# Kernel tuning notes

Measured on AMD Instinct MI355X. Metric: run time of the kernel, lower is better.

The kernel has to match this reference:

```python
import jax, jax.numpy as jnp
import numpy as np

N = 8192
FEAT = 3
TRIG = 2
SA = 2
H = 64
ACT = 3
NEG = -1.0e9
EPS = 1e-5


def setup_inputs() -> dict:
    key = jax.random.key(0)
    ks = jax.random.split(key, 24)
    s = 0.05
    node_features = jax.random.uniform(ks[0], (N, FEAT), dtype=jnp.float32)
    adj = jax.random.randint(ks[1], (N, N), 0, 2).astype(jnp.float32)
    # ensure self-loops so every row has at least one neighbor
    adj_matrix = jnp.maximum(adj, jnp.eye(N, dtype=jnp.float32))
    trigger_context = jax.random.uniform(ks[2], (TRIG,), dtype=jnp.float32)
    sa_priors = jax.random.normal(ks[3], (N, SA), dtype=jnp.float32)
    p = lambda k, sh: jax.random.normal(k, sh, dtype=jnp.float32) * s
    return {
        "node_features": node_features,
        "adj_matrix": adj_matrix,
        "trigger_context": trigger_context,
        "sa_priors": sa_priors,
        # node_encoder: Linear(5,64) -> ReLU -> Linear(64,64)
        "w1": p(ks[4], (FEAT + TRIG, H)), "b1": jnp.zeros((H,), jnp.float32),
        "w2": p(ks[5], (H, H)), "b2": jnp.zeros((H,), jnp.float32),
        "wq": p(ks[6], (H, H)), "bq": jnp.zeros((H,), jnp.float32),
        "wk": p(ks[7], (H, H)), "bk": jnp.zeros((H,), jnp.float32),
        "wg": p(ks[8], (TRIG, H)), "bg": jnp.zeros((H,), jnp.float32),
        "stateful_bias": jnp.zeros((1,), jnp.float32),
        "wm": p(ks[9], (H, H)), "bm": jnp.zeros((H,), jnp.float32),
        "ln_g": jnp.ones((H,), jnp.float32), "ln_b": jnp.zeros((H,), jnp.float32),
        "wa1": p(ks[10], (H + SA, H)), "ba1": jnp.zeros((H,), jnp.float32),
        "wa2": p(ks[11], (H, ACT)), "ba2": jnp.zeros((ACT,), jnp.float32),
    }


def reference(node_features, adj_matrix, trigger_context, sa_priors,
              w1, b1, w2, b2, wq, bq, wk, bk, wg, bg, stateful_bias,
              wm, bm, ln_g, ln_b, wa1, ba1, wa2, ba2):
    n = node_features.shape[0]
    trig = jnp.broadcast_to(trigger_context[None, :], (n, TRIG))
    x = jnp.concatenate([node_features, trig], axis=1)          # [N, 5]
    h = jax.nn.relu(x @ w1 + b1) @ w2 + b2                       # [N, H]
    q = h @ wq + bq
    k = h @ wk + bk
    scores = (q @ k.T) * (1.0 / np.sqrt(H))                      # [N, N]
    gate_factor = jnp.mean(jax.nn.sigmoid(trigger_context @ wg + bg))
    topo = jnp.where(adj_matrix == 0, jnp.float32(NEG), adj_matrix)
    is_stateful = node_features[:, 2]
    is_reactive = 1.0 - trigger_context[0]
    sb = jnp.outer(is_stateful, is_stateful) * (stateful_bias[0] * is_reactive)
    scores = scores * gate_factor + topo + sb
    attn = jax.nn.softmax(scores, axis=1)                        # [N, N]
    messages = h @ wm + bm
    aggregated = attn @ messages                                 # [N, H]
    z = h + aggregated
    mu = jnp.mean(z, axis=-1, keepdims=True)
    var = jnp.mean(jnp.square(z - mu), axis=-1, keepdims=True)
    emb = (z - mu) * jax.lax.rsqrt(var + EPS) * ln_g + ln_b      # LayerNorm
    ai = jnp.concatenate([emb, sa_priors], axis=1)               # [N, H+2]
    q_values = jax.nn.relu(ai @ wa1 + ba1) @ wa2 + ba2           # [N, 3]
    return q_values
```

## Files before the change

kernel.cpp:

```cpp
#include <hip/hip_runtime.h>
#include <hip/hip_bf16.h>
#include <math.h>

#define N 8192
#define NEGV -1000000000.0f
#define EPSV 1e-05f
#define NSPLIT 8
#define CPS (N / NSPLIT)
#define NTILE (CPS / 64)

typedef short bf16x8 __attribute__((ext_vector_type(8)));
typedef float f32x4 __attribute__((ext_vector_type(4)));
typedef unsigned short u16;
typedef unsigned int u32;

#define WS_SCAL 0
#define WS_H    64
#define WS_ST   (WS_H + N * 64)
#define WS_SBI  (WS_ST + N)
#define WS_DEN  (WS_SBI + N)
#define WS_AGG  (WS_DEN + NSPLIT * N)
#define WS_F_END (WS_AGG + NSPLIT * N * 64)
#define WU_BASE (WS_F_END * 2)
#define WU_QB (WU_BASE)
#define WU_KB (WU_BASE + N * 64)
#define WU_MB (WU_BASE + 2 * N * 64)
#define WU_MT (WU_BASE + 3 * N * 64)

static __device__ __forceinline__ u16 f2bf(float f) {
    __hip_bfloat16 h = __float2bfloat16(f);
    return *(u16*)&h;
}
static __device__ __forceinline__ u32 pk2(float a, float b) {
    return (u32)f2bf(a) | ((u32)f2bf(b) << 16);
}

__global__ void prep_k(const float* __restrict__ tc, const float* __restrict__ wg,
                       const float* __restrict__ bg, const float* __restrict__ sbias,
                       float* __restrict__ scal) {
    int j = threadIdx.x;
    float v = tc[0] * wg[j] + tc[1] * wg[64 + j] + bg[j];
    float g = 1.0f / (1.0f + __expf(-v));
    for (int off = 32; off; off >>= 1) g += __shfl_xor(g, off, 64);
    if (j == 0) {
        scal[0] = 0.125f * (g * (1.0f / 64.0f));
        scal[1] = sbias[0] * (1.0f - tc[0]);
    }
}

__global__ __launch_bounds__(256) void embed_k(
    const float* __restrict__ nf, const float* __restrict__ tc,
    const float* __restrict__ w1, const float* __restrict__ b1,
    const float* __restrict__ w2, const float* __restrict__ b2,
    const float* __restrict__ wq, const float* __restrict__ bq,
    const float* __restrict__ wk, const float* __restrict__ bk,
    const float* __restrict__ wm, const float* __restrict__ bm,
    float* __restrict__ ws)
{
    const int w = threadIdx.x >> 6, lane = threadIdx.x & 63;
    const int row = blockIdx.x * 4 + w;
    __shared__ float ts[4][64], hs[4][64];
    const float qscale = ws[WS_SCAL + 0];
    const float coef   = ws[WS_SCAL + 1];
    const float f0 = nf[row * 3], f1 = nf[row * 3 + 1], f2 = nf[row * 3 + 2];
    const float t0 = tc[0], t1 = tc[1];
    float v = b1[lane];
    v = fmaf(f0, w1[lane], v);
    v = fmaf(f1, w1[64 + lane], v);
    v = fmaf(f2, w1[128 + lane], v);
    v = fmaf(t0, w1[192 + lane], v);
    v = fmaf(t1, w1[256 + lane], v);
    ts[w][lane] = fmaxf(v, 0.0f);
    __syncthreads();
    float hv = b2[lane];
    #pragma unroll 8
    for (int j = 0; j < 64; j++) hv = fmaf(ts[w][j], w2[j * 64 + lane], hv);
    hs[w][lane] = hv;
    ws[WS_H + row * 64 + lane] = hv;
    __syncthreads();
    float qv = bq[lane], kv = bk[lane], mv = bm[lane];
    #pragma unroll 4
    for (int j = 0; j < 64; j++) {
        const float hj = hs[w][j];
        qv = fmaf(hj, wq[j * 64 + lane], qv);
        kv = fmaf(hj, wk[j * 64 + lane], kv);
        mv = fmaf(hj, wm[j * 64 + lane], mv);
    }
    u16* wu = (u16*)ws;
    wu[WU_QB + row * 64 + lane] = f2bf(qv * qscale);
    wu[WU_KB + row * 64 + lane] = f2bf(kv);
    wu[WU_MB + row * 64 + lane] = f2bf(mv);
    if (lane == 0) {
        ws[WS_ST + row]  = f2;
        ws[WS_SBI + row] = f2 * coef;
    }
}

__global__ __launch_bounds__(256) void transp_k(float* __restrict__ ws) {
    const u16* mb = (const u16*)ws + WU_MB;
    u16* mt = (u16*)ws + WU_MT;
    __shared__ __align__(16) u16 tile[64][72];
    const int i0 = blockIdx.x * 64;
    const int t = threadIdx.x;
    {
        const int r = t >> 2, cb = (t & 3) * 16;
        *(uint4*)&tile[r][cb]     = *(const uint4*)&mb[(size_t)(i0 + r) * 64 + cb];
        *(uint4*)&tile[r][cb + 8] = *(const uint4*)&mb[(size_t)(i0 + r) * 64 + cb + 8];
    }
    __syncthreads();
    const int c = t >> 2, rb = (t & 3) * 16;
    u16 tmp[16];
    #pragma unroll
    for (int i = 0; i < 16; i++) tmp[i] = tile[rb + i][c];
    *(uint4*)&mt[(size_t)c * N + i0 + rb]     = *(uint4*)&tmp[0];
    *(uint4*)&mt[(size_t)c * N + i0 + rb + 8] = *(uint4*)&tmp[8];
}

__global__ __launch_bounds__(256, 4) void attn_k(const float* __restrict__ adj,
                                                 float* __restrict__ ws)
{
    const int rb = blockIdx.x, sp = blockIdx.y;
    const int i0 = rb * 64, j0 = sp * CPS;
    const int tid = threadIdx.x;
    const int w = tid >> 6, lane = tid & 63;
    const int quad = lane >> 4, n16 = lane & 15;
    const int m0 = w * 16;

    __shared__ __align__(16) u16 ps[4][16][72];

    const u16* qb = (const u16*)ws + WU_QB;
    const u16* kb = (const u16*)ws + WU_KB;
    const u16* mt = (const u16*)ws + WU_MT;

    const u16* qr = qb + (size_t)(i0 + m0 + n16) * 64;
    const bf16x8 aq0 = *(const bf16x8*)&qr[quad * 8];
    const bf16x8 aq1 = *(const bf16x8*)&qr[32 + quad * 8];

    const float sbr = ws[WS_SBI + i0 + m0 + n16];
    const float* adjrow = adj + (size_t)(i0 + m0 + n16) * N;

    f32x4 acc[4];
    #pragma unroll
    for (int i = 0; i < 4; i++) acc[i] = (f32x4){0.f, 0.f, 0.f, 0.f};
    float den = 0.0f;

    f32x4 a4[4];
    #pragma unroll
    for (int ct = 0; ct < 4; ct++)
        a4[ct] = *(const f32x4*)&adjrow[j0 + ct * 16 + quad * 4];

    for (int t = 0; t < NTILE; t++) {
        const int jt = j0 + t * 64;

        f32x4 a4n[4];
        if (t + 1 < NTILE) {
            const int jn = jt + 64;
            #pragma unroll
            for (int ct = 0; ct < 4; ct++)
                a4n[ct] = *(const f32x4*)&adjrow[jn + ct * 16 + quad * 4];
        }

        #pragma unroll
        for (int ct = 0; ct < 4; ct++) {
            const u16* kr = kb + (size_t)(jt + ct * 16 + n16) * 64;
            const bf16x8 k0 = *(const bf16x8*)&kr[quad * 8];
            const bf16x8 k1 = *(const bf16x8*)&kr[32 + quad * 8];
            f32x4 s = {0.f, 0.f, 0.f, 0.f};
            s = __builtin_amdgcn_mfma_f32_16x16x32_bf16(k0, aq0, s, 0, 0, 0);
            s = __builtin_amdgcn_mfma_f32_16x16x32_bf16(k1, aq1, s, 0, 0, 0);
            const f32x4 sv = *(const f32x4*)&ws[WS_ST + jt + ct * 16 + quad * 4];
            const f32x4 av = a4[ct];
            float pv[4];
            #pragma unroll
            for (int r = 0; r < 4; r++) {
                const float e = av[r] * __expf(fmaf(sbr, sv[r], s[r]));
                den += e;
                pv[r] = e;
            }
            *(uint2*)&ps[w][n16][ct * 16 + quad * 4] =
                make_uint2(pk2(pv[0], pv[1]), pk2(pv[2], pv[3]));
        }

        const bf16x8 ap0 = *(const bf16x8*)&ps[w][n16][quad * 8];
        const bf16x8 ap1 = *(const bf16x8*)&ps[w][n16][32 + quad * 8];
        #pragma unroll
        for (int nt = 0; nt < 4; nt++) {
            const u16* mr = mt + (size_t)(nt * 16 + n16) * N + jt;
            const bf16x8 b0 = *(const bf16x8*)&mr[quad * 8];
            const bf16x8 b1 = *(const bf16x8*)&mr[32 + quad * 8];
            acc[nt] = __builtin_amdgcn_mfma_f32_16x16x32_bf16(ap0, b0, acc[nt], 0, 0, 0);
            acc[nt] = __builtin_amdgcn_mfma_f32_16x16x32_bf16(ap1, b1, acc[nt], 0, 0, 0);
        }

        #pragma unroll
        for (int ct = 0; ct < 4; ct++) a4[ct] = a4n[ct];
    }

    float* aggp = ws + WS_AGG + (size_t)sp * N * 64;
    #pragma unroll
    for (int nt = 0; nt < 4; nt++) {
        #pragma unroll
        for (int reg = 0; reg < 4; reg++) {
            aggp[(size_t)(i0 + m0 + quad * 4 + reg) * 64 + nt * 16 + n16] = acc[nt][reg];
        }
    }
    den += __shfl_xor(den, 16, 64);
    den += __shfl_xor(den, 32, 64);
    if (quad == 0) ws[WS_DEN + sp * N + i0 + m0 + n16] = den;
}

__global__ __launch_bounds__(256) void final_k(
    const float* __restrict__ sa, const float* __restrict__ ln_g,
    const float* __restrict__ ln_b,
    const float* __restrict__ wa1, const float* __restrict__ ba1,
    const float* __restrict__ wa2, const float* __restrict__ ba2,
    const float* __restrict__ ws, float* __restrict__ out)
{
    const int w = threadIdx.x >> 6, lane = threadIdx.x & 63;
    const int row = blockIdx.x * 4 + w;
    __shared__ float es[4][64], hs2[4][64];
    float a = 0.0f;
    #pragma unroll
    for (int sp = 0; sp < NSPLIT; sp++)
        a += ws[WS_AGG + (size_t)sp * N * 64 + (size_t)row * 64 + lane];
    float d = 0.0f;
    #pragma unroll
    for (int sp = 0; sp < NSPLIT; sp++) d += ws[WS_DEN + sp * N + row];
    const float z = ws[WS_H + row * 64 + lane] + a / d;
    float mu = z;
    for (int off = 32; off; off >>= 1) mu += __shfl_xor(mu, off, 64);
    mu *= (1.0f / 64.0f);
    const float zc = z - mu;
    float var = zc * zc;
    for (int off = 32; off; off >>= 1) var += __shfl_xor(var, off, 64);
    var *= (1.0f / 64.0f);
    const float emb = zc * rsqrtf(var + EPSV) * ln_g[lane] + ln_b[lane];
    es[w][lane] = emb;
    __syncthreads();
    const float sa0 = sa[row * 2], sa1 = sa[row * 2 + 1];
    float hv = ba1[lane];
    #pragma unroll 8
    for (int c = 0; c < 64; c++) hv = fmaf(es[w][c], wa1[c * 64 + lane], hv);
    hv = fmaf(sa0, wa1[64 * 64 + lane], hv);
    hv = fmaf(sa1, wa1[65 * 64 + lane], hv);
    hs2[w][lane] = fmaxf(hv, 0.0f);
    __syncthreads();
    if (lane < 3) {
        float o = ba2[lane];
        for (int u = 0; u < 64; u++) o = fmaf(hs2[w][u], wa2[u * 3 + lane], o);
        out[row * 3 + lane] = o;
    }
}

extern "C" void kernel_launch(void* const* d_in, const int* in_sizes, int n_in,
                              void* d_out, int out_size, void* d_ws, size_t ws_size,
                              hipStream_t stream)
{
    const float* nf  = (const float*)d_in[0];
    const float* adj = (const float*)d_in[1];
    const float* tc  = (const float*)d_in[2];
    const float* sa  = (const float*)d_in[3];
    const float* w1  = (const float*)d_in[4];
    const float* b1  = (const float*)d_in[5];
    const float* w2  = (const float*)d_in[6];
    const float* b2  = (const float*)d_in[7];
    const float* wq  = (const float*)d_in[8];
    const float* bq  = (const float*)d_in[9];
    const float* wk  = (const float*)d_in[10];
    const float* bk  = (const float*)d_in[11];
    const float* wg  = (const float*)d_in[12];
    const float* bg  = (const float*)d_in[13];
    const float* sb  = (const float*)d_in[14];
    const float* wm  = (const float*)d_in[15];
    const float* bm  = (const float*)d_in[16];
    const float* lng = (const float*)d_in[17];
    const float* lnb = (const float*)d_in[18];
    const float* wa1 = (const float*)d_in[19];
    const float* ba1 = (const float*)d_in[20];
    const float* wa2 = (const float*)d_in[21];
    const float* ba2 = (const float*)d_in[22];
    float* ws  = (float*)d_ws;
    float* out = (float*)d_out;

    prep_k<<<1, 64, 0, stream>>>(tc, wg, bg, sb, ws + WS_SCAL);
    embed_k<<<N / 4, 256, 0, stream>>>(nf, tc, w1, b1, w2, b2, wq, bq, wk, bk,
                                       wm, bm, ws);
    transp_k<<<N / 64, 256, 0, stream>>>(ws);
    attn_k<<<dim3(N / 64, NSPLIT), 256, 0, stream>>>(adj, ws);
    final_k<<<N / 4, 256, 0, stream>>>(sa, lng, lnb, wa1, ba1, wa2, ba2, ws, out);
}
```

Measured before the change: 542.3 us.

## Stage K and message tiles in double-buffered LDS shared by 128-row blocks

The attention kernel now processes 128 query rows per 512-thread block and cooperatively loads each 64-column K tile and transposed-message tile into double-buffered shared memory. The stateful vector slice is also staged once in LDS. This replaces per-wave redundant global/L2 loads of K and messages with shared reuse across 8 waves. The cost is a block-wide barrier every tile, more LDS per block, and fewer blocks in the grid. The kernel is still dominated by streaming the dense fp32 adjacency matrix.

Result: faster. 496.8 us (-8.4%).

```diff
diff --git a/kernel.cpp b/kernel.cpp
--- a/kernel.cpp
+++ b/kernel.cpp
@@ -116,22 +116,33 @@
     *(uint4*)&mt[(size_t)c * N + i0 + rb + 8] = *(uint4*)&tmp[8];
 }
 
-__global__ __launch_bounds__(256, 4) void attn_k(const float* __restrict__ adj,
+__global__ __launch_bounds__(512, 4) void attn_k(const float* __restrict__ adj,
                                                  float* __restrict__ ws)
 {
     const int rb = blockIdx.x, sp = blockIdx.y;
-    const int i0 = rb * 64, j0 = sp * CPS;
+    const int i0 = rb * 128, j0 = sp * CPS;
     const int tid = threadIdx.x;
     const int w = tid >> 6, lane = tid & 63;
     const int quad = lane >> 4, n16 = lane & 15;
     const int m0 = w * 16;
 
-    __shared__ __align__(16) u16 ps[4][16][72];
+    __shared__ __align__(16) u16 ks[2][64][72];
+    __shared__ __align__(16) u16 ms[2][64][72];
+    __shared__ __align__(16) u16 ps[8][16][72];
+    __shared__ float stl[CPS];
 
     const u16* qb = (const u16*)ws + WU_QB;
     const u16* kb = (const u16*)ws + WU_KB;
     const u16* mt = (const u16*)ws + WU_MT;
 
+    const int sr = tid >> 3, scb = (tid & 7) * 8;
+
+    *(uint4*)&ks[0][sr][scb] = *(const uint4*)&kb[(size_t)(j0 + sr) * 64 + scb];
+    *(uint4*)&ms[0][sr][scb] = *(const uint4*)&mt[(size_t)sr * N + j0 + scb];
+    stl[tid]       = ws[WS_ST + j0 + tid];
+    stl[tid + 512] = ws[WS_ST + j0 + tid + 512];
+    __syncthreads();
+
     const u16* qr = qb + (size_t)(i0 + m0 + n16) * 64;
     const bf16x8 aq0 = *(const bf16x8*)&qr[quad * 8];
     const bf16x8 aq1 = *(const bf16x8*)&qr[32 + quad * 8];
@@ -150,11 +161,18 @@
         a4[ct] = *(const f32x4*)&adjrow[j0 + ct * 16 + quad * 4];
 
     for (int t = 0; t < NTILE; t++) {
+        const int cur = t & 1;
         const int jt = j0 + t * 64;
-
+        const bool hn = (t + 1 < NTILE);
+        const int jn = jt + 64;
+
+        uint4 rk, rm;
+        if (hn) {
+            rk = *(const uint4*)&kb[(size_t)(jn + sr) * 64 + scb];
+            rm = *(const uint4*)&mt[(size_t)sr * N + jn + scb];
+        }
         f32x4 a4n[4];
-        if (t + 1 < NTILE) {
-            const int jn = jt + 64;
+        if (hn) {
             #pragma unroll
             for (int ct = 0; ct < 4; ct++)
                 a4n[ct] = *(const f32x4*)&adjrow[jn + ct * 16 + quad * 4];
@@ -162,13 +180,12 @@
 
         #pragma unroll
         for (int ct = 0; ct < 4; ct++) {
-            const u16* kr = kb + (size_t)(jt + ct * 16 + n16) * 64;
-            const bf16x8 k0 = *(const bf16x8*)&kr[quad * 8];
-            const bf16x8 k1 = *(const bf16x8*)&kr[32 + quad * 8];
+            const bf16x8 k0 = *(const bf16x8*)&ks[cur][ct * 16 + n16][quad * 8];
+            const bf16x8 k1 = *(const bf16x8*)&ks[cur][ct * 16 + n16][32 + quad * 8];
             f32x4 s = {0.f, 0.f, 0.f, 0.f};
             s = __builtin_amdgcn_mfma_f32_16x16x32_bf16(k0, aq0, s, 0, 0, 0);
             s = __builtin_amdgcn_mfma_f32_16x16x32_bf16(k1, aq1, s, 0, 0, 0);
-            const f32x4 sv = *(const f32x4*)&ws[WS_ST + jt + ct * 16 + quad * 4];
+            const f32x4 sv = *(const f32x4*)&stl[t * 64 + ct * 16 + quad * 4];
             const f32x4 av = a4[ct];
             float pv[4];
             #pragma unroll
@@ -185,12 +202,17 @@
         const bf16x8 ap1 = *(const bf16x8*)&ps[w][n16][32 + quad * 8];
         #pragma unroll
         for (int nt = 0; nt < 4; nt++) {
-            const u16* mr = mt + (size_t)(nt * 16 + n16) * N + jt;
-            const bf16x8 b0 = *(const bf16x8*)&mr[quad * 8];
-            const bf16x8 b1 = *(const bf16x8*)&mr[32 + quad * 8];
+            const bf16x8 b0 = *(const bf16x8*)&ms[cur][nt * 16 + n16][quad * 8];
+            const bf16x8 b1 = *(const bf16x8*)&ms[cur][nt * 16 + n16][32 + quad * 8];
             acc[nt] = __builtin_amdgcn_mfma_f32_16x16x32_bf16(ap0, b0, acc[nt], 0, 0, 0);
             acc[nt] = __builtin_amdgcn_mfma_f32_16x16x32_bf16(ap1, b1, acc[nt], 0, 0, 0);
         }
+
+        if (hn) {
+            *(uint4*)&ks[cur ^ 1][sr][scb] = rk;
+            *(uint4*)&ms[cur ^ 1][sr][scb] = rm;
+        }
+        __syncthreads();
 
         #pragma unroll
         for (int ct = 0; ct < 4; ct++) a4[ct] = a4n[ct];
@@ -286,6 +308,6 @@
     embed_k<<<N / 4, 256, 0, stream>>>(nf, tc, w1, b1, w2, b2, wq, bq, wk, bk,
                                        wm, bm, ws);
     transp_k<<<N / 64, 256, 0, stream>>>(ws);
-    attn_k<<<dim3(N / 64, NSPLIT), 256, 0, stream>>>(adj, ws);
+    attn_k<<<dim3(N / 128, NSPLIT), 512, 0, stream>>>(adj, ws);
     final_k<<<N / 4, 256, 0, stream>>>(sa, lng, lnb, wa1, ba1, wa2, ba2, ws, out);
 }
```

## Stage K and message tiles in LDS with 32x32 MFMA over 128-row blocks

Applied to the files above, without the earlier changes.

The attention kernel now handles 128 query rows per block. It double-buffers K and transposed-message tiles in shared memory, and the stateful-bias slice sits in LDS too, so each block reuses them instead of every wave reloading them from global memory. Scores and P·M use 32x32x16 bf16 MFMA, and lane shuffles rebuild the P operand in registers rather than round-tripping through LDS. The column split doubles to keep enough blocks in flight, which also doubles the partial aggregate buffers that final_k must write and reduce. That larger workspace footprint may exceed the allocated workspace.

Measured after the change: 467.1 us. 13.9% less time.

```diff
diff --git a/kernel.cpp b/kernel.cpp
--- a/kernel.cpp
+++ b/kernel.cpp
@@ -3,14 +3,14 @@
 #include <math.h>
 
 #define N 8192
-#define NEGV -1000000000.0f
 #define EPSV 1e-05f
-#define NSPLIT 8
+#define NSPLIT 16
 #define CPS (N / NSPLIT)
 #define NTILE (CPS / 64)
 
 typedef short bf16x8 __attribute__((ext_vector_type(8)));
 typedef float f32x4 __attribute__((ext_vector_type(4)));
+typedef float f32x16 __attribute__((ext_vector_type(16)));
 typedef unsigned short u16;
 typedef unsigned int u32;
 
@@ -34,6 +34,13 @@
 static __device__ __forceinline__ u32 pk2(float a, float b) {
     return (u32)f2bf(a) | ((u32)f2bf(b) << 16);
 }
+static __device__ __forceinline__ bf16x8 mk8(u32 a, u32 b, u32 c, u32 d) {
+    union { u32 u[4]; bf16x8 v; } x;
+    x.u[0] = a; x.u[1] = b; x.u[2] = c; x.u[3] = d;
+    return x.v;
+}
+
+#define TILE_BARRIER() asm volatile("s_waitcnt lgkmcnt(0)\n\ts_barrier" ::: "memory")
 
 __global__ void prep_k(const float* __restrict__ tc, const float* __restrict__ wg,
                        const float* __restrict__ bg, const float* __restrict__ sbias,
@@ -120,93 +127,149 @@
                                                  float* __restrict__ ws)
 {
     const int rb = blockIdx.x, sp = blockIdx.y;
-    const int i0 = rb * 64, j0 = sp * CPS;
+    const int i0 = rb * 128, j0 = sp * CPS;
     const int tid = threadIdx.x;
     const int w = tid >> 6, lane = tid & 63;
-    const int quad = lane >> 4, n16 = lane & 15;
-    const int m0 = w * 16;
-
-    __shared__ __align__(16) u16 ps[4][16][72];
-
-    const u16* qb = (const u16*)ws + WU_QB;
-    const u16* kb = (const u16*)ws + WU_KB;
-    const u16* mt = (const u16*)ws + WU_MT;
-
-    const u16* qr = qb + (size_t)(i0 + m0 + n16) * 64;
-    const bf16x8 aq0 = *(const bf16x8*)&qr[quad * 8];
-    const bf16x8 aq1 = *(const bf16x8*)&qr[32 + quad * 8];
-
-    const float sbr = ws[WS_SBI + i0 + m0 + n16];
-    const float* adjrow = adj + (size_t)(i0 + m0 + n16) * N;
-
-    f32x4 acc[4];
-    #pragma unroll
-    for (int i = 0; i < 4; i++) acc[i] = (f32x4){0.f, 0.f, 0.f, 0.f};
+    const int hi = lane >> 5, l31 = lane & 31;
+
+    __shared__ __align__(16) u16 ks[2][64][68];
+    __shared__ __align__(16) u16 ms[2][64][68];
+    __shared__ float stl[CPS];
+
+    const u16* qb  = (const u16*)ws + WU_QB;
+    const u16* kbp = (const u16*)ws + WU_KB;
+    const u16* mtp = (const u16*)ws + WU_MT;
+
+    const int sr = tid >> 2, scb = (tid & 3) * 16;
+
+    *(uint4*)&ks[0][sr][scb]     = *(const uint4*)&kbp[(size_t)(j0 + sr) * 64 + scb];
+    *(uint4*)&ks[0][sr][scb + 8] = *(const uint4*)&kbp[(size_t)(j0 + sr) * 64 + scb + 8];
+    *(uint4*)&ms[0][sr][scb]     = *(const uint4*)&mtp[(size_t)sr * N + j0 + scb];
+    *(uint4*)&ms[0][sr][scb + 8] = *(const uint4*)&mtp[(size_t)sr * N + j0 + scb + 8];
+    stl[tid]       = ws[WS_ST + j0 + tid];
+    stl[tid + 256] = ws[WS_ST + j0 + tid + 256];
+    __syncthreads();
+
+    const int qrow = i0 + w * 32 + l31;
+    const u16* qr = qb + (size_t)qrow * 64;
+    bf16x8 qf[4];
+    #pragma unroll
+    for (int s = 0; s < 4; s++) qf[s] = *(const bf16x8*)&qr[s * 16 + hi * 8];
+
+    const float sbr = ws[WS_SBI + qrow];
+    const float* adjr = adj + (size_t)qrow * N;
+
+    f32x16 acc[2];
+    #pragma unroll
+    for (int hb = 0; hb < 2; hb++)
+        #pragma unroll
+        for (int i = 0; i < 16; i++) acc[hb][i] = 0.0f;
     float den = 0.0f;
 
-    f32x4 a4[4];
-    #pragma unroll
-    for (int ct = 0; ct < 4; ct++)
-        a4[ct] = *(const f32x4*)&adjrow[j0 + ct * 16 + quad * 4];
+    f32x4 av[4];
+    #pragma unroll
+    for (int c2 = 0; c2 < 4; c2++)
+        av[c2] = *(const f32x4*)&adjr[j0 + c2 * 8 + hi * 4];
+
+    uint4 rk0, rk1, rm0, rm1;
 
     for (int t = 0; t < NTILE; t++) {
-        const int jt = j0 + t * 64;
-
-        f32x4 a4n[4];
-        if (t + 1 < NTILE) {
-            const int jn = jt + 64;
-            #pragma unroll
-            for (int ct = 0; ct < 4; ct++)
-                a4n[ct] = *(const f32x4*)&adjrow[jn + ct * 16 + quad * 4];
+        const int cur = t & 1;
+        #pragma unroll
+        for (int kb = 0; kb < 2; kb++) {
+            const int colb = j0 + t * 64 + kb * 32;
+            const int loc  = t * 64 + kb * 32;
+
+            if (kb == 0 && t + 1 < NTILE) {
+                const int jn = j0 + (t + 1) * 64;
+                rk0 = *(const uint4*)&kbp[(size_t)(jn + sr) * 64 + scb];
+                rk1 = *(const uint4*)&kbp[(size_t)(jn + sr) * 64 + scb + 8];
+                rm0 = *(const uint4*)&mtp[(size_t)sr * N + jn + scb];
+                rm1 = *(const uint4*)&mtp[(size_t)sr * N + jn + scb + 8];
+            }
+
+            const bool pn = (2 * t + kb + 1 < 2 * NTILE);
+            f32x4 avn[4];
+            if (pn) {
+                #pragma unroll
+                for (int c2 = 0; c2 < 4; c2++)
+                    avn[c2] = *(const f32x4*)&adjr[colb + 32 + c2 * 8 + hi * 4];
+            } else {
+                #pragma unroll
+                for (int c2 = 0; c2 < 4; c2++) avn[c2] = av[c2];
+            }
+
+            f32x16 d;
+            #pragma unroll
+            for (int i = 0; i < 16; i++) d[i] = 0.0f;
+            #pragma unroll
+            for (int s = 0; s < 4; s++) {
+                const bf16x8 kf = *(const bf16x8*)&ks[cur][kb * 32 + l31][s * 16 + hi * 8];
+                d = __builtin_amdgcn_mfma_f32_32x32x16_bf16(kf, qf[s], d, 0, 0, 0);
+            }
+
+            u32 wlo[4], whi[4];
+            #pragma unroll
+            for (int c2 = 0; c2 < 4; c2++) {
+                const f32x4 sv = *(const f32x4*)&stl[loc + c2 * 8 + hi * 4];
+                const f32x4 a4 = av[c2];
+                const float p0 = a4[0] * __expf(fmaf(sbr, sv[0], d[c2 * 4 + 0]));
+                const float p1 = a4[1] * __expf(fmaf(sbr, sv[1], d[c2 * 4 + 1]));
+                const float p2 = a4[2] * __expf(fmaf(sbr, sv[2], d[c2 * 4 + 2]));
+                const float p3 = a4[3] * __expf(fmaf(sbr, sv[3], d[c2 * 4 + 3]));
+                den += (p0 + p1) + (p2 + p3);
+                wlo[c2] = pk2(p0, p1);
+                whi[c2] = pk2(p2, p3);
+            }
+
+            bf16x8 pa[2];
+            #pragma unroll
+            for (int s2 = 0; s2 < 2; s2++) {
+                const u32 xl0 = (u32)__shfl_xor((int)wlo[2 * s2],     32, 64);
+                const u32 xh0 = (u32)__shfl_xor((int)whi[2 * s2],     32, 64);
+                const u32 xl1 = (u32)__shfl_xor((int)wlo[2 * s2 + 1], 32, 64);
+                const u32 xh1 = (u32)__shfl_xor((int)whi[2 * s2 + 1], 32, 64);
+                const u32 f0 = hi ? xl1 : wlo[2 * s2];
+                const u32 f1 = hi ? xh1 : whi[2 * s2];
+                const u32 f2 = hi ? wlo[2 * s2 + 1] : xl0;
+                const u32 f3 = hi ? whi[2 * s2 + 1] : xh0;
+                pa[s2] = mk8(f0, f1, f2, f3);
+            }
+
+            #pragma unroll
+            for (int hb = 0; hb < 2; hb++) {
+                #pragma unroll
+                for (int s2 = 0; s2 < 2; s2++) {
+                    const bf16x8 mf = *(const bf16x8*)
+                        &ms[cur][hb * 32 + l31][kb * 32 + s2 * 16 + hi * 8];
+                    acc[hb] = __builtin_amdgcn_mfma_f32_32x32x16_bf16(pa[s2], mf, acc[hb], 0, 0, 0);
+                }
+            }
+
+            if (kb == 1 && t + 1 < NTILE) {
+                *(uint4*)&ks[cur ^ 1][sr][scb]     = rk0;
+                *(uint4*)&ks[cur ^ 1][sr][scb + 8] = rk1;
+                *(uint4*)&ms[cur ^ 1][sr][scb]     = rm0;
+                *(uint4*)&ms[cur ^ 1][sr][scb + 8] = rm1;
+            }
+
+            #pragma unroll
+            for (int c2 = 0; c2 < 4; c2++) av[c2] = avn[c2];
         }
-
+        if (t + 1 < NTILE) TILE_BARRIER();
+    }
+
+    float* aggp = ws + WS_AGG + (size_t)sp * N * 64;
+    #pragma unroll
+    for (int hb = 0; hb < 2; hb++) {
         #pragma unroll
-        for (int ct = 0; ct < 4; ct++) {
-            const u16* kr = kb + (size_t)(jt + ct * 16 + n16) * 64;
-            const bf16x8 k0 = *(const bf16x8*)&kr[quad * 8];
-            const bf16x8 k1 = *(const bf16x8*)&kr[32 + quad * 8];
-            f32x4 s = {0.f, 0.f, 0.f, 0.f};
-            s = __builtin_amdgcn_mfma_f32_16x16x32_bf16(k0, aq0, s, 0, 0, 0);
-            s = __builtin_amdgcn_mfma_f32_16x16x32_bf16(k1, aq1, s, 0, 0, 0);
-            const f32x4 sv = *(const f32x4*)&ws[WS_ST + jt + ct * 16 + quad * 4];
-            const f32x4 av = a4[ct];
-            float pv[4];
-            #pragma unroll
-            for (int r = 0; r < 4; r++) {
-                const float e = av[r] * __expf(fmaf(sbr, sv[r], s[r]));
-                den += e;
-                pv[r] = e;
-            }
-            *(uint2*)&ps[w][n16][ct * 16 + quad * 4] =
-                make_uint2(pk2(pv[0], pv[1]), pk2(pv[2], pv[3]));
+        for (int reg = 0; reg < 16; reg++) {
+            const int qv = (reg & 3) + 8 * (reg >> 2) + 4 * hi;
+            aggp[(size_t)(i0 + w * 32 + qv) * 64 + hb * 32 + l31] = acc[hb][reg];
         }
-
-        const bf16x8 ap0 = *(const bf16x8*)&ps[w][n16][quad * 8];
-        const bf16x8 ap1 = *(const bf16x8*)&ps[w][n16][32 + quad * 8];
-        #pragma unroll
-        for (int nt = 0; nt < 4; nt++) {
-            const u16* mr = mt + (size_t)(nt * 16 + n16) * N + jt;
-            const bf16x8 b0 = *(const bf16x8*)&mr[quad * 8];
-            const bf16x8 b1 = *(const bf16x8*)&mr[32 + quad * 8];
-            acc[nt] = __builtin_amdgcn_mfma_f32_16x16x32_bf16(ap0, b0, acc[nt], 0, 0, 0);
-            acc[nt] = __builtin_amdgcn_mfma_f32_16x16x32_bf16(ap1, b1, acc[nt], 0, 0, 0);
-        }
-
-        #pragma unroll
-        for (int ct = 0; ct < 4; ct++) a4[ct] = a4n[ct];
-    }
-
-    float* aggp = ws + WS_AGG + (size_t)sp * N * 64;
-    #pragma unroll
-    for (int nt = 0; nt < 4; nt++) {
-        #pragma unroll
-        for (int reg = 0; reg < 4; reg++) {
-            aggp[(size_t)(i0 + m0 + quad * 4 + reg) * 64 + nt * 16 + n16] = acc[nt][reg];
-        }
-    }
-    den += __shfl_xor(den, 16, 64);
+    }
     den += __shfl_xor(den, 32, 64);
-    if (quad == 0) ws[WS_DEN + sp * N + i0 + m0 + n16] = den;
+    if (hi == 0) ws[WS_DEN + sp * N + i0 + w * 32 + l31] = den;
 }
 
 __global__ __launch_bounds__(256) void final_k(
@@ -286,6 +349,6 @@
     embed_k<<<N / 4, 256, 0, stream>>>(nf, tc, w1, b1, w2, b2, wq, bq, wk, bk,
                                        wm, bm, ws);
     transp_k<<<N / 64, 256, 0, stream>>>(ws);
-    attn_k<<<dim3(N / 64, NSPLIT), 256, 0, stream>>>(adj, ws);
+    attn_k<<<dim3(N / 128, NSPLIT), 256, 0, stream>>>(adj, ws);
     final_k<<<N / 4, 256, 0, stream>>>(sa, lng, lnb, wa1, ba1, wa2, ba2, ws, out);
 }
```
